# Kernel tuning notes

Measured on AMD Instinct MI355X. Metric: run time of the kernel, lower is better.

The kernel has to match this reference:

```python
import jax, jax.numpy as jnp
import numpy as np

NUM_HEADS = 16


def setup_inputs() -> dict:
    key = jax.random.key(0)
    ks = jax.random.split(key, 8)
    B_, N, C = 2048, 64, 512
    nW = 64
    return {
        "x": jax.random.normal(ks[0], (B_, N, C), dtype=jnp.float32),
        "pe": jax.random.normal(ks[1], (1, N, C), dtype=jnp.float32),
        "rpe": jax.random.normal(ks[2], (NUM_HEADS, N, N), dtype=jnp.float32),
        "mask": jax.random.normal(ks[3], (nW, N, N), dtype=jnp.float32),
        "qkv_w": jax.random.normal(ks[4], (3 * C, C), dtype=jnp.float32) * 0.02,
        "qkv_b": jax.random.normal(ks[5], (3 * C,), dtype=jnp.float32) * 0.02,
        "proj_w": jax.random.normal(ks[6], (C, C), dtype=jnp.float32) * 0.02,
        "proj_b": jax.random.normal(ks[7], (C,), dtype=jnp.float32) * 0.02,
    }


def reference(x, pe, rpe, mask, qkv_w, qkv_b, proj_w, proj_b):
    B_, N, C = x.shape
    H = NUM_HEADS
    hd = C // H
    scale = hd ** -0.5
    xp = x + pe  # (B_, N, C)
    qkv = xp @ qkv_w.T + qkv_b  # (B_, N, 3C)
    qkv = qkv.reshape(B_, N, 3, H, hd).transpose(2, 0, 3, 1, 4)  # (3, B_, H, N, hd)
    q, k, v = qkv[0], qkv[1], qkv[2]
    attn = jnp.einsum("bhnd,bhmd->bhnm", q * scale, k)  # (B_, H, N, N)
    attn = attn + rpe[None]  # broadcast rpe over batch
    nW = mask.shape[0]
    attn = attn.reshape(B_ // nW, nW, H, N, N) + mask[None, :, None]
    attn = attn.reshape(B_, H, N, N)
    attn = jax.nn.softmax(attn, axis=-1)
    out = jnp.einsum("bhnm,bhmd->bhnd", attn, v)  # (B_, H, N, hd)
    out = out.transpose(0, 2, 1, 3).reshape(B_, N, C)
    return out @ proj_w.T + proj_b
```

## Files before the change

kernel.cpp:

```cpp
#include <hip/hip_runtime.h>
#include <hip/hip_bf16.h>
#include <cstdint>

typedef __bf16 bf16;
typedef __bf16 bf16x8_t __attribute__((ext_vector_type(8)));
typedef __bf16 bf16x4_t __attribute__((ext_vector_type(4)));
typedef float  f32x4_t  __attribute__((ext_vector_type(4)));

#define MFMA16(a, b, c) __builtin_amdgcn_mfma_f32_16x16x32_bf16((a), (b), (c), 0, 0, 0)

__device__ __forceinline__ void gload_lds16(const bf16* g, bf16* l) {
    __builtin_amdgcn_global_load_lds(
        (const __attribute__((address_space(1))) void*)g,
        (__attribute__((address_space(3))) void*)l,
        16, 0, 0);
}

__global__ void k_wprep(const float* __restrict__ wq, const float* __restrict__ wp,
                        bf16* __restrict__ wqb, bf16* __restrict__ wpb) {
    int t = blockIdx.x * 256 + threadIdx.x;
    int stride = gridDim.x * 256;
    for (int i = t; i < 196608; i += stride) {
        float4 v = ((const float4*)wq)[i];
        bf16x4_t o; o[0]=(bf16)v.x; o[1]=(bf16)v.y; o[2]=(bf16)v.z; o[3]=(bf16)v.w;
        ((bf16x4_t*)wqb)[i] = o;
    }
    for (int i = t; i < 65536; i += stride) {
        float4 v = ((const float4*)wp)[i];
        bf16x4_t o; o[0]=(bf16)v.x; o[1]=(bf16)v.y; o[2]=(bf16)v.z; o[3]=(bf16)v.w;
        ((bf16x4_t*)wpb)[i] = o;
    }
}

__global__ void k_xprep(const float* __restrict__ x, const float* __restrict__ pe,
                        bf16* __restrict__ xp) {
    int t = blockIdx.x * 256 + threadIdx.x;
    int stride = gridDim.x * 256;
    for (int i = t; i < 8388608; i += stride) {
        int row = i >> 6;
        int g   = (i & 63) * 8;
        const float* xr = x  + ((size_t)row << 9) + g;
        const float* pr = pe + ((size_t)(row & 63) << 9) + g;
        float4 x0 = *(const float4*)(xr);
        float4 x1 = *(const float4*)(xr + 4);
        float4 p0 = *(const float4*)(pr);
        float4 p1 = *(const float4*)(pr + 4);
        bf16x8_t v;
        v[0]=(bf16)(x0.x+p0.x); v[1]=(bf16)(x0.y+p0.y);
        v[2]=(bf16)(x0.z+p0.z); v[3]=(bf16)(x0.w+p0.w);
        v[4]=(bf16)(x1.x+p1.x); v[5]=(bf16)(x1.y+p1.y);
        v[6]=(bf16)(x1.z+p1.z); v[7]=(bf16)(x1.w+p1.w);
        *(bf16x8_t*)(xp + (size_t)i * 8) = v;
    }
}

__global__ __launch_bounds__(256, 2) void k_qkv(
    const bf16*  __restrict__ A,
    const bf16*  __restrict__ Bw,
    const float* __restrict__ bias,
    bf16* __restrict__ Cq)
{
    __shared__ bf16 As[2][128 * 64];
    __shared__ bf16 Bs[2][128 * 64];

    const int tid  = threadIdx.x;
    const int lane = tid & 63;
    const int wave = tid >> 6;
    const int lr = lane & 15, lg = lane >> 4;
    const int wr = wave >> 1, wc = wave & 1;
    const int bid = blockIdx.x;
    const int wg  = (bid & 7) * 384 + (bid >> 3);
    const int mb  = wg / 12, nb = wg - mb * 12;
    const size_t m0 = (size_t)mb * 128;
    const int n0 = nb * 128;

    f32x4_t acc[4][4] = {};

    auto stage = [&](int kt, int buf) {
        const int k0 = kt * 64;
#pragma unroll
        for (int ii = 0; ii < 4; ++ii) {
            int instr = wave * 4 + ii;
            int r  = instr * 8 + (lane >> 3);
            int gp = (lane & 7) ^ (r & 7);
            gload_lds16(A  + (m0 + r) * 512 + k0 + gp * 8, &As[buf][instr * 512]);
            gload_lds16(Bw + (size_t)(n0 + r) * 512 + k0 + gp * 8, &Bs[buf][instr * 512]);
        }
    };

    stage(0, 0);

    for (int kt = 0; kt < 8; ++kt) {
        const int cur = kt & 1;
        if (kt < 7) {
            stage(kt + 1, cur ^ 1);
            asm volatile("s_waitcnt vmcnt(8) lgkmcnt(0)" ::: "memory");
        } else {
            asm volatile("s_waitcnt vmcnt(0) lgkmcnt(0)" ::: "memory");
        }
        __builtin_amdgcn_sched_barrier(0);
        __builtin_amdgcn_s_barrier();
        __builtin_amdgcn_sched_barrier(0);

#pragma unroll
        for (int k2 = 0; k2 < 2; ++k2) {
            bf16x8_t af[4], bfr[4];
#pragma unroll
            for (int i = 0; i < 4; ++i) {
                int rowa = wr * 64 + i * 16 + lr;
                int ph   = (k2 * 4 + lg) ^ (rowa & 7);
                af[i] = *(const bf16x8_t*)&As[cur][rowa * 64 + ph * 8];
            }
#pragma unroll
            for (int j = 0; j < 4; ++j) {
                int rowb = wc * 64 + j * 16 + lr;
                int ph   = (k2 * 4 + lg) ^ (rowb & 7);
                bfr[j] = *(const bf16x8_t*)&Bs[cur][rowb * 64 + ph * 8];
            }
#pragma unroll
            for (int i = 0; i < 4; ++i)
#pragma unroll
                for (int j = 0; j < 4; ++j)
                    acc[i][j] = MFMA16(af[i], bfr[j], acc[i][j]);
        }

        if (kt < 7) {
            asm volatile("s_waitcnt lgkmcnt(0)" ::: "memory");
            __builtin_amdgcn_sched_barrier(0);
            __builtin_amdgcn_s_barrier();
            __builtin_amdgcn_sched_barrier(0);
        }
    }

    float bj[4];
#pragma unroll
    for (int j = 0; j < 4; ++j) bj[j] = bias[n0 + wc * 64 + j * 16 + lr];
#pragma unroll
    for (int i = 0; i < 4; ++i)
#pragma unroll
        for (int j = 0; j < 4; ++j) {
            int col   = n0 + wc * 64 + j * 16 + lr;
            int which = col >> 9;
            int h     = (col >> 5) & 15;
            int d     = col & 31;
            bf16* base = Cq + (size_t)(which * 16 + h) * (512 * 2048);
#pragma unroll
            for (int r = 0; r < 4; ++r) {
                int mrow = (int)m0 + wr * 64 + i * 16 + lg * 4 + r;
                int win = mrow >> 6, tok = mrow & 63;
                base[(size_t)win * 2048 + tok * 32 + d] = (bf16)(acc[i][j][r] + bj[j]);
            }
        }
}

__global__ __launch_bounds__(256, 2) void k_attn(
    const bf16*  __restrict__ qkv,
    const float* __restrict__ rpe,
    const float* __restrict__ mask,
    bf16* __restrict__ ao,
    int winbase)
{
    __shared__ bf16 vts[4][32 * 72];
    __shared__ bf16 ps[4][64 * 72];

    const int tid  = threadIdx.x;
    const int lane = tid & 63;
    const int wave = tid >> 6;
    const int lr   = lane & 15;
    const int lg   = lane >> 4;
    const int bw   = blockIdx.x;
    const int gw   = winbase + bw;
    const int wi   = gw & 63;
    const float* mp = mask + (size_t)wi * 4096;
    bf16* pvt = &vts[wave][0];
    bf16* pps = &ps[wave][0];

    const float SCALE = 0.17677669529663687f;

    for (int hh = 0; hh < 4; ++hh) {
        const int h  = wave * 4 + hh;
        const float* rp = rpe + (size_t)h * 4096;
        const bf16* qb = qkv + ((size_t)(h)      * 512 + bw) * 2048;
        const bf16* kb = qkv + ((size_t)(16 + h) * 512 + bw) * 2048;
        const bf16* vb = qkv + ((size_t)(32 + h) * 512 + bw) * 2048;

        bf16x8_t qf[4], kf[4];
#pragma unroll
        for (int t = 0; t < 4; ++t) {
            qf[t] = *(const bf16x8_t*)(qb + (t * 16 + lr) * 32 + lg * 8);
            kf[t] = *(const bf16x8_t*)(kb + (t * 16 + lr) * 32 + lg * 8);
        }
#pragma unroll
        for (int j = 0; j < 4; ++j) {
            bf16x8_t vr = *(const bf16x8_t*)(vb + (j * 16 + (lane >> 2)) * 32 + (lane & 3) * 8);
#pragma unroll
            for (int i = 0; i < 8; ++i)
                pvt[((lane & 3) * 8 + i) * 72 + j * 16 + (lane >> 2)] = vr[i];
        }

        float sminv[4][4];
#pragma unroll
        for (int mt = 0; mt < 4; ++mt) {
            f32x4_t s[4];
            f32x4_t zero = {};
#pragma unroll
            for (int nt = 0; nt < 4; ++nt)
                s[nt] = MFMA16(qf[mt], kf[nt], zero);
            float rm[4][4];
#pragma unroll
            for (int nt = 0; nt < 4; ++nt) {
                int col = nt * 16 + lr;
#pragma unroll
                for (int r = 0; r < 4; ++r) {
                    int rrow = mt * 16 + lg * 4 + r;
                    rm[nt][r] = rp[rrow * 64 + col] + mp[rrow * 64 + col];
                }
            }
            float mx[4] = {-1e30f, -1e30f, -1e30f, -1e30f};
#pragma unroll
            for (int nt = 0; nt < 4; ++nt)
#pragma unroll
                for (int r = 0; r < 4; ++r) {
                    float tv = s[nt][r] * SCALE + rm[nt][r];
                    s[nt][r] = tv;
                    mx[r] = fmaxf(mx[r], tv);
                }
#pragma unroll
            for (int r = 0; r < 4; ++r) {
                float m = mx[r];
                m = fmaxf(m, __shfl_xor(m, 1));
                m = fmaxf(m, __shfl_xor(m, 2));
                m = fmaxf(m, __shfl_xor(m, 4));
                m = fmaxf(m, __shfl_xor(m, 8));
                mx[r] = m;
            }
            float sm[4] = {0.f, 0.f, 0.f, 0.f};
#pragma unroll
            for (int nt = 0; nt < 4; ++nt)
#pragma unroll
                for (int r = 0; r < 4; ++r) {
                    float e = __expf(s[nt][r] - mx[r]);
                    s[nt][r] = e;
                    sm[r] += e;
                }
#pragma unroll
            for (int r = 0; r < 4; ++r) {
                float ssum = sm[r];
                ssum += __shfl_xor(ssum, 1);
                ssum += __shfl_xor(ssum, 2);
                ssum += __shfl_xor(ssum, 4);
                ssum += __shfl_xor(ssum, 8);
                sminv[mt][r] = 1.0f / ssum;
            }
#pragma unroll
            for (int nt = 0; nt < 4; ++nt)
#pragma unroll
                for (int r = 0; r < 4; ++r)
                    pps[(mt * 16 + lg * 4 + r) * 72 + nt * 16 + lr] = (bf16)s[nt][r];
        }

#pragma unroll
        for (int mt = 0; mt < 4; ++mt) {
            f32x4_t o[2] = {};
#pragma unroll
            for (int ks = 0; ks < 2; ++ks) {
                bf16x8_t pa = *(const bf16x8_t*)&pps[(mt * 16 + lr) * 72 + ks * 32 + lg * 8];
#pragma unroll
                for (int jd = 0; jd < 2; ++jd) {
                    bf16x8_t bv = *(const bf16x8_t*)&pvt[(jd * 16 + lr) * 72 + ks * 32 + lg * 8];
                    o[jd] = MFMA16(pa, bv, o[jd]);
                }
            }
#pragma unroll
            for (int jd = 0; jd < 2; ++jd)
#pragma unroll
                for (int r = 0; r < 4; ++r) {
                    size_t rrow = (size_t)gw * 64 + mt * 16 + lg * 4 + r;
                    ao[rrow * 512 + h * 32 + jd * 16 + lr] = (bf16)(o[jd][r] * sminv[mt][r]);
                }
        }
    }
}

__global__ __launch_bounds__(256, 2) void k_proj(
    const bf16* __restrict__ A, const bf16* __restrict__ Bw,
    const float* __restrict__ bias, float* __restrict__ C)
{
    __shared__ bf16 As[2][128 * 64];
    __shared__ bf16 Bs[2][128 * 64];

    const int tid  = threadIdx.x;
    const int lane = tid & 63;
    const int wave = tid >> 6;
    const int lr = lane & 15, lg = lane >> 4;
    const int wr = wave >> 1, wc = wave & 1;
    const int bid = blockIdx.x;
    const int wg  = (bid & 7) * 512 + (bid >> 3);
    const int mb = wg >> 2, nb = wg & 3;
    const size_t m0 = (size_t)mb * 128;
    const int n0 = nb * 128;

    f32x4_t acc[4][4] = {};

    auto stage = [&](int kt, int buf) {
        const int k0 = kt * 64;
#pragma unroll
        for (int ii = 0; ii < 4; ++ii) {
            int instr = wave * 4 + ii;
            int r  = instr * 8 + (lane >> 3);
            int gp = (lane & 7) ^ (r & 7);
            gload_lds16(A  + (m0 + r) * 512 + k0 + gp * 8, &As[buf][instr * 512]);
            gload_lds16(Bw + (size_t)(n0 + r) * 512 + k0 + gp * 8, &Bs[buf][instr * 512]);
        }
    };

    stage(0, 0);

    for (int kt = 0; kt < 8; ++kt) {
        const int cur = kt & 1;
        if (kt < 7) {
            stage(kt + 1, cur ^ 1);
            asm volatile("s_waitcnt vmcnt(8) lgkmcnt(0)" ::: "memory");
        } else {
            asm volatile("s_waitcnt vmcnt(0) lgkmcnt(0)" ::: "memory");
        }
        __builtin_amdgcn_sched_barrier(0);
        __builtin_amdgcn_s_barrier();
        __builtin_amdgcn_sched_barrier(0);

#pragma unroll
        for (int k2 = 0; k2 < 2; ++k2) {
            bf16x8_t af[4], bfr[4];
#pragma unroll
            for (int i = 0; i < 4; ++i) {
                int rowa = wr * 64 + i * 16 + lr;
                int ph   = (k2 * 4 + lg) ^ (rowa & 7);
                af[i] = *(const bf16x8_t*)&As[cur][rowa * 64 + ph * 8];
            }
#pragma unroll
            for (int j = 0; j < 4; ++j) {
                int rowb = wc * 64 + j * 16 + lr;
                int ph   = (k2 * 4 + lg) ^ (rowb & 7);
                bfr[j] = *(const bf16x8_t*)&Bs[cur][rowb * 64 + ph * 8];
            }
#pragma unroll
            for (int i = 0; i < 4; ++i)
#pragma unroll
                for (int j = 0; j < 4; ++j)
                    acc[i][j] = MFMA16(af[i], bfr[j], acc[i][j]);
        }

        if (kt < 7) {
            asm volatile("s_waitcnt lgkmcnt(0)" ::: "memory");
            __builtin_amdgcn_sched_barrier(0);
            __builtin_amdgcn_s_barrier();
            __builtin_amdgcn_sched_barrier(0);
        }
    }

    float bj[4];
#pragma unroll
    for (int j = 0; j < 4; ++j) bj[j] = bias[n0 + wc * 64 + j * 16 + lr];
#pragma unroll
    for (int i = 0; i < 4; ++i)
#pragma unroll
        for (int j = 0; j < 4; ++j) {
            int col = n0 + wc * 64 + j * 16 + lr;
#pragma unroll
            for (int r = 0; r < 4; ++r) {
                size_t rw = m0 + wr * 64 + i * 16 + lg * 4 + r;
                C[rw * 512 + col] = acc[i][j][r] + bj[j];
            }
        }
}

extern "C" void kernel_launch(void* const* d_in, const int* in_sizes, int n_in,
                              void* d_out, int out_size, void* d_ws, size_t ws_size,
                              hipStream_t stream) {
    (void)in_sizes; (void)n_in; (void)out_size; (void)ws_size;
    const float* x      = (const float*)d_in[0];
    const float* pe     = (const float*)d_in[1];
    const float* rpe    = (const float*)d_in[2];
    const float* mask   = (const float*)d_in[3];
    const float* qkv_w  = (const float*)d_in[4];
    const float* qkv_b  = (const float*)d_in[5];
    const float* proj_w = (const float*)d_in[6];
    const float* proj_b = (const float*)d_in[7];
    float* out = (float*)d_out;

    char* ws = (char*)d_ws;
    bf16* wqkvb  = (bf16*)ws;
    bf16* wprojb = (bf16*)(ws + 1572864);
    bf16* ao     = (bf16*)(ws + 2097152);

    bf16* xp   = (bf16*)d_out;
    bf16* qkvc = (bf16*)((char*)d_out + 134217728);

    k_wprep<<<256, 256, 0, stream>>>(qkv_w, proj_w, wqkvb, wprojb);
    k_xprep<<<4096, 256, 0, stream>>>(x, pe, xp);
    for (int c = 0; c < 4; ++c) {
        k_qkv<<<3072, 256, 0, stream>>>(xp + (size_t)c * 32768 * 512,
                                        wqkvb, qkv_b, qkvc);
        k_attn<<<512, 256, 0, stream>>>(qkvc, rpe, mask, ao, c * 512);
    }
    k_proj<<<4096, 256, 0, stream>>>(ao, wprojb, proj_b, out);
}
```

Before: 784.9 us.

## Drop LDS double buffering in GEMMs to raise occupancy to four blocks

Both the QKV and projection GEMM kernels go from a double-buffered LDS pipeline with hand-placed waitcnt/barrier sequences to a single 32KB buffer with plain __syncthreads around each k-step. Launch bounds go from 2 to 4 blocks per CU. The aim is to hide global-load latency through more resident waves rather than software prefetch. The cost is that loads are no longer overlapped with MFMA work inside a block, and the higher occupancy bound may force register spills given the 64-float accumulator array.

```diff
diff --git a/kernel.cpp b/kernel.cpp
--- a/kernel.cpp
+++ b/kernel.cpp
@@ -54,14 +54,14 @@
     }
 }
 
-__global__ __launch_bounds__(256, 2) void k_qkv(
+__global__ __launch_bounds__(256, 4) void k_qkv(
     const bf16*  __restrict__ A,
     const bf16*  __restrict__ Bw,
     const float* __restrict__ bias,
     bf16* __restrict__ Cq)
 {
-    __shared__ bf16 As[2][128 * 64];
-    __shared__ bf16 Bs[2][128 * 64];
+    __shared__ bf16 As[128 * 64];
+    __shared__ bf16 Bs[128 * 64];
 
     const int tid  = threadIdx.x;
     const int lane = tid & 63;
@@ -76,31 +76,17 @@
 
     f32x4_t acc[4][4] = {};
 
-    auto stage = [&](int kt, int buf) {
+    for (int kt = 0; kt < 8; ++kt) {
         const int k0 = kt * 64;
 #pragma unroll
         for (int ii = 0; ii < 4; ++ii) {
             int instr = wave * 4 + ii;
             int r  = instr * 8 + (lane >> 3);
             int gp = (lane & 7) ^ (r & 7);
-            gload_lds16(A  + (m0 + r) * 512 + k0 + gp * 8, &As[buf][instr * 512]);
-            gload_lds16(Bw + (size_t)(n0 + r) * 512 + k0 + gp * 8, &Bs[buf][instr * 512]);
-        }
-    };
-
-    stage(0, 0);
-
-    for (int kt = 0; kt < 8; ++kt) {
-        const int cur = kt & 1;
-        if (kt < 7) {
-            stage(kt + 1, cur ^ 1);
-            asm volatile("s_waitcnt vmcnt(8) lgkmcnt(0)" ::: "memory");
-        } else {
-            asm volatile("s_waitcnt vmcnt(0) lgkmcnt(0)" ::: "memory");
-        }
-        __builtin_amdgcn_sched_barrier(0);
-        __builtin_amdgcn_s_barrier();
-        __builtin_amdgcn_sched_barrier(0);
+            gload_lds16(A  + (m0 + r) * 512 + k0 + gp * 8, &As[instr * 512]);
+            gload_lds16(Bw + (size_t)(n0 + r) * 512 + k0 + gp * 8, &Bs[instr * 512]);
+        }
+        __syncthreads();
 
 #pragma unroll
         for (int k2 = 0; k2 < 2; ++k2) {
@@ -109,13 +95,13 @@
             for (int i = 0; i < 4; ++i) {
                 int rowa = wr * 64 + i * 16 + lr;
                 int ph   = (k2 * 4 + lg) ^ (rowa & 7);
-                af[i] = *(const bf16x8_t*)&As[cur][rowa * 64 + ph * 8];
+                af[i] = *(const bf16x8_t*)&As[rowa * 64 + ph * 8];
             }
 #pragma unroll
             for (int j = 0; j < 4; ++j) {
                 int rowb = wc * 64 + j * 16 + lr;
                 int ph   = (k2 * 4 + lg) ^ (rowb & 7);
-                bfr[j] = *(const bf16x8_t*)&Bs[cur][rowb * 64 + ph * 8];
+                bfr[j] = *(const bf16x8_t*)&Bs[rowb * 64 + ph * 8];
             }
 #pragma unroll
             for (int i = 0; i < 4; ++i)
@@ -123,13 +109,7 @@
                 for (int j = 0; j < 4; ++j)
                     acc[i][j] = MFMA16(af[i], bfr[j], acc[i][j]);
         }
-
-        if (kt < 7) {
-            asm volatile("s_waitcnt lgkmcnt(0)" ::: "memory");
-            __builtin_amdgcn_sched_barrier(0);
-            __builtin_amdgcn_s_barrier();
-            __builtin_amdgcn_sched_barrier(0);
-        }
+        __syncthreads();
     }
 
     float bj[4];
@@ -282,12 +262,12 @@
     }
 }
 
-__global__ __launch_bounds__(256, 2) void k_proj(
+__global__ __launch_bounds__(256, 4) void k_proj(
     const bf16* __restrict__ A, const bf16* __restrict__ Bw,
     const float* __restrict__ bias, float* __restrict__ C)
 {
-    __shared__ bf16 As[2][128 * 64];
-    __shared__ bf16 Bs[2][128 * 64];
+    __shared__ bf16 As[128 * 64];
+    __shared__ bf16 Bs[128 * 64];
 
     const int tid  = threadIdx.x;
     const int lane = tid & 63;
@@ -302,31 +282,17 @@
 
     f32x4_t acc[4][4] = {};
 
-    auto stage = [&](int kt, int buf) {
+    for (int kt = 0; kt < 8; ++kt) {
         const int k0 = kt * 64;
 #pragma unroll
         for (int ii = 0; ii < 4; ++ii) {
             int instr = wave * 4 + ii;
             int r  = instr * 8 + (lane >> 3);
             int gp = (lane & 7) ^ (r & 7);
-            gload_lds16(A  + (m0 + r) * 512 + k0 + gp * 8, &As[buf][instr * 512]);
-            gload_lds16(Bw + (size_t)(n0 + r) * 512 + k0 + gp * 8, &Bs[buf][instr * 512]);
-        }
-    };
-
-    stage(0, 0);
-
-    for (int kt = 0; kt < 8; ++kt) {
-        const int cur = kt & 1;
-        if (kt < 7) {
-            stage(kt + 1, cur ^ 1);
-            asm volatile("s_waitcnt vmcnt(8) lgkmcnt(0)" ::: "memory");
-        } else {
-            asm volatile("s_waitcnt vmcnt(0) lgkmcnt(0)" ::: "memory");
-        }
-        __builtin_amdgcn_sched_barrier(0);
-        __builtin_amdgcn_s_barrier();
-        __builtin_amdgcn_sched_barrier(0);
+            gload_lds16(A  + (m0 + r) * 512 + k0 + gp * 8, &As[instr * 512]);
+            gload_lds16(Bw + (size_t)(n0 + r) * 512 + k0 + gp * 8, &Bs[instr * 512]);
+        }
+        __syncthreads();
 
 #pragma unroll
         for (int k2 = 0; k2 < 2; ++k2) {
@@ -335,13 +301,13 @@
             for (int i = 0; i < 4; ++i) {
                 int rowa = wr * 64 + i * 16 + lr;
                 int ph   = (k2 * 4 + lg) ^ (rowa & 7);
-                af[i] = *(const bf16x8_t*)&As[cur][rowa * 64 + ph * 8];
+                af[i] = *(const bf16x8_t*)&As[rowa * 64 + ph * 8];
             }
 #pragma unroll
             for (int j = 0; j < 4; ++j) {
                 int rowb = wc * 64 + j * 16 + lr;
                 int ph   = (k2 * 4 + lg) ^ (rowb & 7);
-                bfr[j] = *(const bf16x8_t*)&Bs[cur][rowb * 64 + ph * 8];
+                bfr[j] = *(const bf16x8_t*)&Bs[rowb * 64 + ph * 8];
             }
 #pragma unroll
             for (int i = 0; i < 4; ++i)
@@ -349,13 +315,7 @@
                 for (int j = 0; j < 4; ++j)
                     acc[i][j] = MFMA16(af[i], bfr[j], acc[i][j]);
         }
-
-        if (kt < 7) {
-            asm volatile("s_waitcnt lgkmcnt(0)" ::: "memory");
-            __builtin_amdgcn_sched_barrier(0);
-            __builtin_amdgcn_s_barrier();
-            __builtin_amdgcn_sched_barrier(0);
-        }
+        __syncthreads();
     }
 
     float bj[4];
```

After: 712.3 us. 1.1x faster.
